# Kernel optimization log

Hardware: AMD Instinct MI355X
Metric: run time of the kernel (lower is better)

Reference implementation:

```python
import jax, jax.numpy as jnp
import numpy as np

B, H, S, D = 8, 16, 1024, 64

def setup_inputs() -> dict:
    key = jax.random.key(0)
    k1, k2, k3, k4 = jax.random.split(key, 4)
    Q = jax.random.normal(k1, (B, H, S, D), dtype=jnp.float32)
    K = jax.random.normal(k2, (B, H, S, D), dtype=jnp.float32)
    V = jax.random.normal(k3, (B, H, S, D), dtype=jnp.float32)
    mask = jax.random.randint(k4, (B,), 0, 2).astype(jnp.bool_)
    return {"Q": Q, "K": K, "V": V, "mask": mask}

def reference(Q, K, V, mask):
    # scores: [B,H,S,S]
    scores = jnp.einsum('bhqd,bhkd->bhqk', Q, K)
    # per-batch-element mask broadcast over heads and both seq dims
    scores = jnp.where(mask[:, None, None, None], jnp.float32(-1e9), scores)
    # NOTE: original divides by sqrt(d) AFTER masking, so masked value is -1e9/sqrt(d)
    inv_sqrt_d = jnp.float32(1.0 / np.sqrt(Q.shape[-1]))
    attn = jax.nn.softmax(scores * inv_sqrt_d, axis=-1)
    return jnp.einsum('bhqk,bhkd->bhqd', attn, V)
```

## Files before the change

### kernel.cpp

```cpp
#include <hip/hip_runtime.h>
#include <hip/hip_bf16.h>

typedef __bf16 bf16;
typedef __bf16 bf16x4 __attribute__((ext_vector_type(4)));
typedef __bf16 bf16x8 __attribute__((ext_vector_type(8)));
typedef float  f32x16 __attribute__((ext_vector_type(16)));

#define S_  1024
#define D_  64
#define BQ  128
#define BK  64
#define KT  (S_/BK)
#define QT  (S_/BQ)
#define LD  72

#define ZERO16 {0.f,0.f,0.f,0.f,0.f,0.f,0.f,0.f,0.f,0.f,0.f,0.f,0.f,0.f,0.f,0.f}

__global__ __launch_bounds__(256, 4)
void fa_fwd(const float* __restrict__ Q, const float* __restrict__ K,
            const float* __restrict__ V, const int* __restrict__ mask,
            float* __restrict__ O)
{
    __shared__ bf16 ks[BK][LD];
    __shared__ bf16 vt[D_][LD];
    __shared__ bf16 ps[4][32][LD];

    const int tid  = threadIdx.x;
    const int lane = tid & 63;
    const int w    = tid >> 6;
    const int l32  = lane & 31;
    const int hi   = lane >> 5;

    const int bid   = blockIdx.x;
    const int xcd   = bid & 7;
    const int rnd   = bid >> 3;
    const int qtile = rnd & 7;
    const int bh    = ((rnd >> 3) << 3) | xcd;
    const int b     = bh >> 4;
    const size_t base = (size_t)bh * (S_ * D_);
    const int qW = qtile * BQ + w * 32;

    const float qscale = (mask[b] != 0) ? 0.0f : 0.1803368801111204f;

    bf16x8 qf[4];
    {
        const float* qp = Q + base + (size_t)(qW + l32) * D_ + hi * 8;
        #pragma unroll
        for (int kc = 0; kc < 4; ++kc) {
            float4 a = *(const float4*)(qp + kc * 16);
            float4 c = *(const float4*)(qp + kc * 16 + 4);
            bf16x8 f;
            f[0] = (bf16)(a.x * qscale); f[1] = (bf16)(a.y * qscale);
            f[2] = (bf16)(a.z * qscale); f[3] = (bf16)(a.w * qscale);
            f[4] = (bf16)(c.x * qscale); f[5] = (bf16)(c.y * qscale);
            f[6] = (bf16)(c.z * qscale); f[7] = (bf16)(c.w * qscale);
            qf[kc] = f;
        }
    }

    f32x16 o0 = ZERO16, o1 = ZERO16;
    float lsum = 0.f;

    const int vkq = (tid >> 2) & 15;
    const int vc4 = (tid & 3) + 4 * w;
    const float4* gk = (const float4*)(K + base);
    const float4* gv = (const float4*)(V + base);
    bf16* psw = &ps[w][l32][0];

    float4 kr[4], vr[4];
    #pragma unroll
    for (int it = 0; it < 4; ++it)
        kr[it] = gk[it * 256 + tid];
    #pragma unroll
    for (int r = 0; r < 4; ++r)
        vr[r] = gv[(vkq * 4 + r) * 16 + vc4];

    for (int kt = 0; kt < KT; ++kt) {
        __syncthreads();
        #pragma unroll
        for (int it = 0; it < 4; ++it) {
            int i = it * 256 + tid;
            int row = i >> 4, c4 = i & 15;
            bf16x4 hk = {(bf16)kr[it].x, (bf16)kr[it].y, (bf16)kr[it].z, (bf16)kr[it].w};
            *(bf16x4*)&ks[row][c4 * 4] = hk;
        }
        {
            bf16x4 t0 = {(bf16)vr[0].x, (bf16)vr[1].x, (bf16)vr[2].x, (bf16)vr[3].x};
            bf16x4 t1 = {(bf16)vr[0].y, (bf16)vr[1].y, (bf16)vr[2].y, (bf16)vr[3].y};
            bf16x4 t2 = {(bf16)vr[0].z, (bf16)vr[1].z, (bf16)vr[2].z, (bf16)vr[3].z};
            bf16x4 t3 = {(bf16)vr[0].w, (bf16)vr[1].w, (bf16)vr[2].w, (bf16)vr[3].w};
            *(bf16x4*)&vt[vc4 * 4 + 0][vkq * 4] = t0;
            *(bf16x4*)&vt[vc4 * 4 + 1][vkq * 4] = t1;
            *(bf16x4*)&vt[vc4 * 4 + 2][vkq * 4] = t2;
            *(bf16x4*)&vt[vc4 * 4 + 3][vkq * 4] = t3;
        }
        __syncthreads();

        {
            int ktn = (kt + 1 < KT) ? (kt + 1) : kt;
            #pragma unroll
            for (int it = 0; it < 4; ++it)
                kr[it] = gk[ktn * 1024 + it * 256 + tid];
            #pragma unroll
            for (int r = 0; r < 4; ++r)
                vr[r] = gv[ktn * 1024 + (vkq * 4 + r) * 16 + vc4];
        }

        f32x16 s0 = ZERO16, s1 = ZERO16;
        #pragma unroll
        for (int kc = 0; kc < 4; ++kc) {
            bf16x8 k0 = *(const bf16x8*)&ks[l32][kc * 16 + hi * 8];
            bf16x8 k1 = *(const bf16x8*)&ks[32 + l32][kc * 16 + hi * 8];
            s0 = __builtin_amdgcn_mfma_f32_32x32x16_bf16(k0, qf[kc], s0, 0, 0, 0);
            s1 = __builtin_amdgcn_mfma_f32_32x32x16_bf16(k1, qf[kc], s1, 0, 0, 0);
        }

        #pragma unroll
        for (int g = 0; g < 4; ++g) {
            bf16x4 p0, p1;
            #pragma unroll
            for (int r = 0; r < 4; ++r) {
                float e0 = __builtin_amdgcn_exp2f(s0[g * 4 + r]);
                float e1 = __builtin_amdgcn_exp2f(s1[g * 4 + r]);
                lsum += e0 + e1;
                p0[r] = (bf16)e0;
                p1[r] = (bf16)e1;
            }
            *(bf16x4*)&psw[g * 8 + hi * 4]      = p0;
            *(bf16x4*)&psw[32 + g * 8 + hi * 4] = p1;
        }

        #pragma unroll
        for (int kc = 0; kc < 4; ++kc) {
            bf16x8 pf = *(const bf16x8*)&psw[kc * 16 + hi * 8];
            bf16x8 v0 = *(const bf16x8*)&vt[l32][kc * 16 + hi * 8];
            bf16x8 v1 = *(const bf16x8*)&vt[32 + l32][kc * 16 + hi * 8];
            o0 = __builtin_amdgcn_mfma_f32_32x32x16_bf16(v0, pf, o0, 0, 0, 0);
            o1 = __builtin_amdgcn_mfma_f32_32x32x16_bf16(v1, pf, o1, 0, 0, 0);
        }
    }

    lsum += __shfl_xor(lsum, 32);
    float inv = 1.0f / lsum;
    float* op = O + base + (size_t)(qW + l32) * D_ + hi * 4;
    #pragma unroll
    for (int g = 0; g < 4; ++g) {
        float4 a = { o0[g * 4 + 0] * inv, o0[g * 4 + 1] * inv,
                     o0[g * 4 + 2] * inv, o0[g * 4 + 3] * inv };
        *(float4*)(op + g * 8) = a;
        float4 c = { o1[g * 4 + 0] * inv, o1[g * 4 + 1] * inv,
                     o1[g * 4 + 2] * inv, o1[g * 4 + 3] * inv };
        *(float4*)(op + 32 + g * 8) = c;
    }
}

extern "C" void kernel_launch(void* const* d_in, const int* in_sizes, int n_in,
                              void* d_out, int out_size, void* d_ws, size_t ws_size,
                              hipStream_t stream)
{
    const float* Q    = (const float*)d_in[0];
    const float* K    = (const float*)d_in[1];
    const float* V    = (const float*)d_in[2];
    const int*   mask = (const int*)d_in[3];
    float*       O    = (float*)d_out;

    dim3 grid(8 * 16 * QT);
    fa_fwd<<<grid, 256, 0, stream>>>(Q, K, V, mask, O);
}
```

Before: 164.9 us.

## Double Q rows per warp, keep P in registers, double-buffer K/V LDS

```diff
diff --git a/kernel.cpp b/kernel.cpp
--- a/kernel.cpp
+++ b/kernel.cpp
@@ -8,7 +8,7 @@
 
 #define S_  1024
 #define D_  64
-#define BQ  128
+#define BQ  256
 #define BK  64
 #define KT  (S_/BK)
 #define QT  (S_/BQ)
@@ -16,14 +16,13 @@
 
 #define ZERO16 {0.f,0.f,0.f,0.f,0.f,0.f,0.f,0.f,0.f,0.f,0.f,0.f,0.f,0.f,0.f,0.f}
 
-__global__ __launch_bounds__(256, 4)
+__global__ __launch_bounds__(256, 2)
 void fa_fwd(const float* __restrict__ Q, const float* __restrict__ K,
             const float* __restrict__ V, const int* __restrict__ mask,
             float* __restrict__ O)
 {
-    __shared__ bf16 ks[BK][LD];
-    __shared__ bf16 vt[D_][LD];
-    __shared__ bf16 ps[4][32][LD];
+    __shared__ bf16 ks[2][BK][LD];
+    __shared__ bf16 vt[2][D_][LD];
 
     const int tid  = threadIdx.x;
     const int lane = tid & 63;
@@ -34,17 +33,18 @@
     const int bid   = blockIdx.x;
     const int xcd   = bid & 7;
     const int rnd   = bid >> 3;
-    const int qtile = rnd & 7;
-    const int bh    = ((rnd >> 3) << 3) | xcd;
+    const int qtile = rnd & 3;
+    const int bh    = ((rnd >> 2) << 3) | xcd;
     const int b     = bh >> 4;
     const size_t base = (size_t)bh * (S_ * D_);
-    const int qW = qtile * BQ + w * 32;
+    const int qW = qtile * BQ + w * 64;
 
     const float qscale = (mask[b] != 0) ? 0.0f : 0.1803368801111204f;
 
-    bf16x8 qf[4];
-    {
-        const float* qp = Q + base + (size_t)(qW + l32) * D_ + hi * 8;
+    bf16x8 qf[2][4];
+    #pragma unroll
+    for (int nt = 0; nt < 2; ++nt) {
+        const float* qp = Q + base + (size_t)(qW + nt * 32 + l32) * D_ + hi * 8;
         #pragma unroll
         for (int kc = 0; kc < 4; ++kc) {
             float4 a = *(const float4*)(qp + kc * 16);
@@ -54,103 +54,114 @@
             f[2] = (bf16)(a.z * qscale); f[3] = (bf16)(a.w * qscale);
             f[4] = (bf16)(c.x * qscale); f[5] = (bf16)(c.y * qscale);
             f[6] = (bf16)(c.z * qscale); f[7] = (bf16)(c.w * qscale);
-            qf[kc] = f;
+            qf[nt][kc] = f;
         }
     }
 
-    f32x16 o0 = ZERO16, o1 = ZERO16;
-    float lsum = 0.f;
+    f32x16 o[2][2];
+    #pragma unroll
+    for (int dm = 0; dm < 2; ++dm)
+        #pragma unroll
+        for (int nt = 0; nt < 2; ++nt) o[dm][nt] = (f32x16)ZERO16;
+    float lsum[2] = {0.f, 0.f};
 
     const int vkq = (tid >> 2) & 15;
+    const int vkp = (vkq & 12) | ((vkq & 1) << 1) | ((vkq >> 1) & 1);
     const int vc4 = (tid & 3) + 4 * w;
     const float4* gk = (const float4*)(K + base);
     const float4* gv = (const float4*)(V + base);
-    bf16* psw = &ps[w][l32][0];
 
     float4 kr[4], vr[4];
     #pragma unroll
-    for (int it = 0; it < 4; ++it)
-        kr[it] = gk[it * 256 + tid];
+    for (int it = 0; it < 4; ++it) kr[it] = gk[it * 256 + tid];
     #pragma unroll
-    for (int r = 0; r < 4; ++r)
-        vr[r] = gv[(vkq * 4 + r) * 16 + vc4];
+    for (int r = 0; r < 4; ++r)    vr[r]  = gv[(vkq * 4 + r) * 16 + vc4];
+
+    auto mkpf = [&](const f32x16& sv, bf16x8& fA, bf16x8& fB, float& ls) {
+        bf16x8 a, c;
+        #pragma unroll
+        for (int i = 0; i < 8; ++i) {
+            float e0 = __builtin_amdgcn_exp2f(sv[i]);
+            float e1 = __builtin_amdgcn_exp2f(sv[8 + i]);
+            ls += e0 + e1;
+            a[i] = (bf16)e0;
+            c[i] = (bf16)e1;
+        }
+        fA = a; fB = c;
+    };
 
     for (int kt = 0; kt < KT; ++kt) {
-        __syncthreads();
+        bf16 (*ksb)[LD] = ks[kt & 1];
+        bf16 (*vtb)[LD] = vt[kt & 1];
+
         #pragma unroll
         for (int it = 0; it < 4; ++it) {
             int i = it * 256 + tid;
             int row = i >> 4, c4 = i & 15;
             bf16x4 hk = {(bf16)kr[it].x, (bf16)kr[it].y, (bf16)kr[it].z, (bf16)kr[it].w};
-            *(bf16x4*)&ks[row][c4 * 4] = hk;
+            *(bf16x4*)&ksb[row][c4 * 4] = hk;
         }
         {
             bf16x4 t0 = {(bf16)vr[0].x, (bf16)vr[1].x, (bf16)vr[2].x, (bf16)vr[3].x};
             bf16x4 t1 = {(bf16)vr[0].y, (bf16)vr[1].y, (bf16)vr[2].y, (bf16)vr[3].y};
             bf16x4 t2 = {(bf16)vr[0].z, (bf16)vr[1].z, (bf16)vr[2].z, (bf16)vr[3].z};
             bf16x4 t3 = {(bf16)vr[0].w, (bf16)vr[1].w, (bf16)vr[2].w, (bf16)vr[3].w};
-            *(bf16x4*)&vt[vc4 * 4 + 0][vkq * 4] = t0;
-            *(bf16x4*)&vt[vc4 * 4 + 1][vkq * 4] = t1;
-            *(bf16x4*)&vt[vc4 * 4 + 2][vkq * 4] = t2;
-            *(bf16x4*)&vt[vc4 * 4 + 3][vkq * 4] = t3;
+            *(bf16x4*)&vtb[vc4 * 4 + 0][vkp * 4] = t0;
+            *(bf16x4*)&vtb[vc4 * 4 + 1][vkp * 4] = t1;
+            *(bf16x4*)&vtb[vc4 * 4 + 2][vkp * 4] = t2;
+            *(bf16x4*)&vtb[vc4 * 4 + 3][vkp * 4] = t3;
+        }
+        {
+            int ktn = (kt + 1 < KT) ? (kt + 1) : kt;
+            #pragma unroll
+            for (int it = 0; it < 4; ++it) kr[it] = gk[ktn * 1024 + it * 256 + tid];
+            #pragma unroll
+            for (int r = 0; r < 4; ++r)    vr[r]  = gv[ktn * 1024 + (vkq * 4 + r) * 16 + vc4];
         }
         __syncthreads();
 
-        {
-            int ktn = (kt + 1 < KT) ? (kt + 1) : kt;
-            #pragma unroll
-            for (int it = 0; it < 4; ++it)
-                kr[it] = gk[ktn * 1024 + it * 256 + tid];
-            #pragma unroll
-            for (int r = 0; r < 4; ++r)
-                vr[r] = gv[ktn * 1024 + (vkq * 4 + r) * 16 + vc4];
+        f32x16 s00 = ZERO16, s01 = ZERO16, s10 = ZERO16, s11 = ZERO16;
+        #pragma unroll
+        for (int kc = 0; kc < 4; ++kc) {
+            bf16x8 k0 = *(const bf16x8*)&ksb[l32][kc * 16 + hi * 8];
+            bf16x8 k1 = *(const bf16x8*)&ksb[32 + l32][kc * 16 + hi * 8];
+            s00 = __builtin_amdgcn_mfma_f32_32x32x16_bf16(k0, qf[0][kc], s00, 0, 0, 0);
+            s01 = __builtin_amdgcn_mfma_f32_32x32x16_bf16(k0, qf[1][kc], s01, 0, 0, 0);
+            s10 = __builtin_amdgcn_mfma_f32_32x32x16_bf16(k1, qf[0][kc], s10, 0, 0, 0);
+            s11 = __builtin_amdgcn_mfma_f32_32x32x16_bf16(k1, qf[1][kc], s11, 0, 0, 0);
         }
 
-        f32x16 s0 = ZERO16, s1 = ZERO16;
-        #pragma unroll
-        for (int kc = 0; kc < 4; ++kc) {
-            bf16x8 k0 = *(const bf16x8*)&ks[l32][kc * 16 + hi * 8];
-            bf16x8 k1 = *(const bf16x8*)&ks[32 + l32][kc * 16 + hi * 8];
-            s0 = __builtin_amdgcn_mfma_f32_32x32x16_bf16(k0, qf[kc], s0, 0, 0, 0);
-            s1 = __builtin_amdgcn_mfma_f32_32x32x16_bf16(k1, qf[kc], s1, 0, 0, 0);
-        }
-
-        #pragma unroll
-        for (int g = 0; g < 4; ++g) {
-            bf16x4 p0, p1;
-            #pragma unroll
-            for (int r = 0; r < 4; ++r) {
-                float e0 = __builtin_amdgcn_exp2f(s0[g * 4 + r]);
-                float e1 = __builtin_amdgcn_exp2f(s1[g * 4 + r]);
-                lsum += e0 + e1;
-                p0[r] = (bf16)e0;
-                p1[r] = (bf16)e1;
-            }
-            *(bf16x4*)&psw[g * 8 + hi * 4]      = p0;
-            *(bf16x4*)&psw[32 + g * 8 + hi * 4] = p1;
-        }
+        bf16x8 pf[4][2];
+        mkpf(s00, pf[0][0], pf[1][0], lsum[0]);
+        mkpf(s01, pf[0][1], pf[1][1], lsum[1]);
+        mkpf(s10, pf[2][0], pf[3][0], lsum[0]);
+        mkpf(s11, pf[2][1], pf[3][1], lsum[1]);
 
         #pragma unroll
         for (int kc = 0; kc < 4; ++kc) {
-            bf16x8 pf = *(const bf16x8*)&psw[kc * 16 + hi * 8];
-            bf16x8 v0 = *(const bf16x8*)&vt[l32][kc * 16 + hi * 8];
-            bf16x8 v1 = *(const bf16x8*)&vt[32 + l32][kc * 16 + hi * 8];
-            o0 = __builtin_amdgcn_mfma_f32_32x32x16_bf16(v0, pf, o0, 0, 0, 0);
-            o1 = __builtin_amdgcn_mfma_f32_32x32x16_bf16(v1, pf, o1, 0, 0, 0);
+            bf16x8 v0 = *(const bf16x8*)&vtb[l32][kc * 16 + hi * 8];
+            bf16x8 v1 = *(const bf16x8*)&vtb[32 + l32][kc * 16 + hi * 8];
+            o[0][0] = __builtin_amdgcn_mfma_f32_32x32x16_bf16(v0, pf[kc][0], o[0][0], 0, 0, 0);
+            o[0][1] = __builtin_amdgcn_mfma_f32_32x32x16_bf16(v0, pf[kc][1], o[0][1], 0, 0, 0);
+            o[1][0] = __builtin_amdgcn_mfma_f32_32x32x16_bf16(v1, pf[kc][0], o[1][0], 0, 0, 0);
+            o[1][1] = __builtin_amdgcn_mfma_f32_32x32x16_bf16(v1, pf[kc][1], o[1][1], 0, 0, 0);
         }
     }
 
-    lsum += __shfl_xor(lsum, 32);
-    float inv = 1.0f / lsum;
-    float* op = O + base + (size_t)(qW + l32) * D_ + hi * 4;
     #pragma unroll
-    for (int g = 0; g < 4; ++g) {
-        float4 a = { o0[g * 4 + 0] * inv, o0[g * 4 + 1] * inv,
-                     o0[g * 4 + 2] * inv, o0[g * 4 + 3] * inv };
-        *(float4*)(op + g * 8) = a;
-        float4 c = { o1[g * 4 + 0] * inv, o1[g * 4 + 1] * inv,
-                     o1[g * 4 + 2] * inv, o1[g * 4 + 3] * inv };
-        *(float4*)(op + 32 + g * 8) = c;
+    for (int nt = 0; nt < 2; ++nt) {
+        float lv = lsum[nt] + __shfl_xor(lsum[nt], 32);
+        float inv = 1.0f / lv;
+        float* op = O + base + (size_t)(qW + nt * 32 + l32) * D_ + hi * 4;
+        #pragma unroll
+        for (int g = 0; g < 4; ++g) {
+            float4 a = { o[0][nt][g * 4 + 0] * inv, o[0][nt][g * 4 + 1] * inv,
+                         o[0][nt][g * 4 + 2] * inv, o[0][nt][g * 4 + 3] * inv };
+            *(float4*)(op + g * 8) = a;
+            float4 c = { o[1][nt][g * 4 + 0] * inv, o[1][nt][g * 4 + 1] * inv,
+                         o[1][nt][g * 4 + 2] * inv, o[1][nt][g * 4 + 3] * inv };
+            *(float4*)(op + 32 + g * 8) = c;
+        }
     }
 }
 
```

After: 150.0 us. 9.0% less time.
